# Kernel optimization log

Hardware: AMD Instinct MI355X
Metric: run time of the kernel (lower is better)

## Reference

```python
import jax, jax.numpy as jnp
import numpy as np

NUM_HEADS = 4
SCALE = 0.1767766952966369  # head_dim**-0.5, head_dim=32


def setup_inputs() -> dict:
    key = jax.random.key(0)
    k1, k2, k3 = jax.random.split(key, 3)
    B, N, C = 4096, 49, 384  # B = 64 images * 64 windows, N = 7*7, C = 3*embed_dims
    qkv = jax.random.normal(k1, (B, N, C), dtype=jnp.float32)
    mask = jax.random.normal(k2, (NUM_HEADS, N, N), dtype=jnp.float32)
    rotate_mask = jax.random.normal(k3, (64, N, N), dtype=jnp.float32)  # nW = 64
    hw_pad = jnp.array([56, 56], dtype=jnp.int32)  # metadata only, unused in math
    return {"qkv": qkv, "mask": mask, "rotate_mask": rotate_mask, "hw_pad": hw_pad}


def reference(qkv, mask, rotate_mask, hw_pad):
    B, N, C = qkv.shape
    H = NUM_HEADS
    hd = C // H // 3
    # [B,N,3,H,hd] -> [3,B,H,N,hd]
    qkv_r = qkv.reshape(B, N, 3, H, hd).transpose(2, 0, 3, 1, 4)
    q, k, v = qkv_r[0] * SCALE, qkv_r[1], qkv_r[2]
    attn = jnp.einsum('bhqd,bhkd->bhqk', q, k) + mask  # mask broadcasts over B
    nW = rotate_mask.shape[0]
    # shifted-window mask: add per-window rotate mask, broadcast over image batch and heads
    attn = attn.reshape(B // nW, nW, H, N, N) + rotate_mask[None, :, None, :, :]
    attn = jax.nn.softmax(attn.reshape(B, H, N, N), axis=-1)
    out = jnp.einsum('bhqk,bhkd->bhqd', attn, v)  # [B,H,N,hd]
    return out.transpose(0, 2, 1, 3).reshape(B, N, C // 3)
```

## Files before the change

### kernel.cpp

```cpp
#include <hip/hip_runtime.h>

#define NTOK 49
#define NH 4
#define HD 32
#define CIN 384
#define NW 64
#define NPAD 64
#define SCALE_F 0.1767766952966369f

typedef _Float16 f16x8 __attribute__((ext_vector_type(8)));
typedef float f32x16 __attribute__((ext_vector_type(16)));
typedef __fp16 fp16x2 __attribute__((ext_vector_type(2)));

__device__ __forceinline__ unsigned int pkh(float a, float b) {
    fp16x2 h = __builtin_amdgcn_cvt_pkrtz(a, b);
    return __builtin_bit_cast(unsigned int, h);
}

__global__ __launch_bounds__(64) void prep_cmask(
    const float* __restrict__ mask,
    const float* __restrict__ rot,
    float* __restrict__ cmT)
{
    const int wh = blockIdx.x;
    const int w = wh >> 2, h = wh & 3;
    const int i = threadIdx.x;
    for (int j = 0; j < NPAD; ++j) {
        float v;
        if (j >= NTOK) v = -1e30f;
        else if (i >= NTOK) v = 0.f;
        else v = mask[(h * NTOK + i) * NTOK + j] + rot[(w * NTOK + i) * NTOK + j];
        cmT[((size_t)wh * NPAD + j) * NPAD + i] = v;
    }
}

template<bool USE_CM>
__global__ __launch_bounds__(64) void win_attn_mfma(
    const float* __restrict__ qkv,
    const float* __restrict__ mask,
    const float* __restrict__ rot,
    const float* __restrict__ cmT,
    float* __restrict__ out)
{
    const int h = blockIdx.x & 3;
    const int b = blockIdx.x >> 2;
    const int w = b & (NW - 1);
    const int lane = threadIdx.x;
    const int l31 = lane & 31;
    const int hl = lane >> 5;

    __shared__ _Float16 Qs[NPAD * HD];
    __shared__ _Float16 Ks[NPAD * HD];

    const float* base = qkv + (size_t)b * (NTOK * CIN) + h * HD;

    #pragma unroll
    for (int t8 = 0; t8 < 8; ++t8) {
        const int idx = lane + t8 * 64;
        const int n = idx >> 3;
        const int c = idx & 7;
        float4 fq = make_float4(0.f, 0.f, 0.f, 0.f);
        float4 fk = fq;
        if (n < NTOK) {
            const float* p = base + n * CIN + c * 4;
            fq = *reinterpret_cast<const float4*>(p);
            fk = *reinterpret_cast<const float4*>(p + 128);
        }
        uint2 uq, uk;
        uq.x = pkh(fq.x * SCALE_F, fq.y * SCALE_F);
        uq.y = pkh(fq.z * SCALE_F, fq.w * SCALE_F);
        uk.x = pkh(fk.x, fk.y);
        uk.y = pkh(fk.z, fk.w);
        *reinterpret_cast<uint2*>(&Qs[n * HD + c * 4]) = uq;
        *reinterpret_cast<uint2*>(&Ks[n * HD + c * 4]) = uk;
    }

    float cm[2][2][16];
    #pragma unroll
    for (int it = 0; it < 2; ++it) {
        #pragma unroll
        for (int jt = 0; jt < 2; ++jt) {
            #pragma unroll
            for (int r = 0; r < 16; ++r) {
                const int j = (r & 3) + 8 * (r >> 2) + 4 * hl + 32 * jt;
                const int i = l31 + 32 * it;
                if (USE_CM) {
                    cm[it][jt][r] = cmT[((size_t)(w * 4 + h) * NPAD + j) * NPAD + i];
                } else {
                    float v;
                    if (j >= NTOK) v = -1e30f;
                    else if (i >= NTOK) v = 0.f;
                    else v = mask[(h * NTOK + i) * NTOK + j] + rot[(w * NTOK + i) * NTOK + j];
                    cm[it][jt][r] = v;
                }
            }
        }
    }

    __syncthreads();

    f16x8 ka[2][2], qa[2][2];
    #pragma unroll
    for (int t = 0; t < 2; ++t) {
        #pragma unroll
        for (int ks = 0; ks < 2; ++ks) {
            ka[t][ks] = *reinterpret_cast<const f16x8*>(&Ks[(l31 + 32 * t) * HD + ks * 16 + hl * 8]);
            qa[t][ks] = *reinterpret_cast<const f16x8*>(&Qs[(l31 + 32 * t) * HD + ks * 16 + hl * 8]);
        }
    }

    f32x16 acc[2][2];
    #pragma unroll
    for (int it = 0; it < 2; ++it) {
        #pragma unroll
        for (int jt = 0; jt < 2; ++jt) {
            f32x16 a;
            #pragma unroll
            for (int r = 0; r < 16; ++r) a[r] = 0.f;
            a = __builtin_amdgcn_mfma_f32_32x32x16_f16(ka[jt][0], qa[it][0], a, 0, 0, 0);
            a = __builtin_amdgcn_mfma_f32_32x32x16_f16(ka[jt][1], qa[it][1], a, 0, 0, 0);
            acc[it][jt] = a;
        }
    }

    #pragma unroll
    for (int it = 0; it < 2; ++it) {
        float m = -3e38f;
        #pragma unroll
        for (int jt = 0; jt < 2; ++jt) {
            #pragma unroll
            for (int r = 0; r < 16; ++r) {
                acc[it][jt][r] += cm[it][jt][r];
                m = fmaxf(m, acc[it][jt][r]);
            }
        }
        m = fmaxf(m, __shfl_xor(m, 32));
        float s = 0.f;
        #pragma unroll
        for (int jt = 0; jt < 2; ++jt) {
            #pragma unroll
            for (int r = 0; r < 16; ++r) {
                const float e = __expf(acc[it][jt][r] - m);
                acc[it][jt][r] = e;
                s += e;
            }
        }
        s += __shfl_xor(s, 32);
        const float inv = 1.f / s;
        #pragma unroll
        for (int jt = 0; jt < 2; ++jt) {
            #pragma unroll
            for (int r = 0; r < 16; ++r)
                acc[it][jt][r] *= inv;
        }
    }

    f32x16 oacc[2];
    #pragma unroll
    for (int it = 0; it < 2; ++it) {
        #pragma unroll
        for (int r = 0; r < 16; ++r) oacc[it][r] = 0.f;
    }

    #pragma unroll
    for (int ks = 0; ks < 4; ++ks) {
        unsigned int vd[4];
        #pragma unroll
        for (int ep = 0; ep < 4; ++ep) {
            const int j0 = 16 * ks + 8 * hl + 2 * ep;
            float v0 = 0.f, v1 = 0.f;
            if (j0 < NTOK)
                v0 = qkv[((size_t)b * NTOK + j0) * CIN + 256 + h * HD + l31];
            if (j0 + 1 < NTOK)
                v1 = qkv[((size_t)b * NTOK + j0 + 1) * CIN + 256 + h * HD + l31];
            vd[ep] = pkh(v0, v1);
        }
        uint4 vu = make_uint4(vd[0], vd[1], vd[2], vd[3]);
        const f16x8 vb = __builtin_bit_cast(f16x8, vu);

        const int jt = ks >> 1;
        const int r8 = 8 * (ks & 1);
        #pragma unroll
        for (int it = 0; it < 2; ++it) {
            const unsigned int lo0 = pkh(acc[it][jt][r8 + 0], acc[it][jt][r8 + 1]);
            const unsigned int lo1 = pkh(acc[it][jt][r8 + 2], acc[it][jt][r8 + 3]);
            const unsigned int hi0 = pkh(acc[it][jt][r8 + 4], acc[it][jt][r8 + 5]);
            const unsigned int hi1 = pkh(acc[it][jt][r8 + 6], acc[it][jt][r8 + 7]);
            const unsigned int x0 = hl ? lo0 : hi0;
            const unsigned int x1 = hl ? lo1 : hi1;
            const unsigned int y0 = (unsigned int)__shfl_xor((int)x0, 32);
            const unsigned int y1 = (unsigned int)__shfl_xor((int)x1, 32);
            uint4 pu;
            pu.x = hl ? y0 : lo0;
            pu.y = hl ? y1 : lo1;
            pu.z = hl ? hi0 : y0;
            pu.w = hl ? hi1 : y1;
            const f16x8 pa = __builtin_bit_cast(f16x8, pu);
            oacc[it] = __builtin_amdgcn_mfma_f32_32x32x16_f16(pa, vb, oacc[it], 0, 0, 0);
        }
    }

    #pragma unroll
    for (int it = 0; it < 2; ++it) {
        #pragma unroll
        for (int r = 0; r < 16; ++r) {
            const int i = (r & 3) + 8 * (r >> 2) + 4 * hl + 32 * it;
            if (i < NTOK)
                out[((size_t)b * NTOK + i) * (NH * HD) + h * HD + l31] = oacc[it][r];
        }
    }
}

extern "C" void kernel_launch(void* const* d_in, const int* in_sizes, int n_in,
                              void* d_out, int out_size, void* d_ws, size_t ws_size,
                              hipStream_t stream) {
    const float* qkv  = (const float*)d_in[0];
    const float* mask = (const float*)d_in[1];
    const float* rot  = (const float*)d_in[2];
    float* out = (float*)d_out;

    const int Btot = in_sizes[0] / (NTOK * CIN);
    dim3 grid(Btot * NH);

    const size_t cm_bytes = (size_t)NW * NH * NPAD * NPAD * sizeof(float);
    if (ws_size >= cm_bytes && d_ws != nullptr) {
        float* cmT = (float*)d_ws;
        prep_cmask<<<dim3(NW * NH), 64, 0, stream>>>(mask, rot, cmT);
        win_attn_mfma<true><<<grid, 64, 0, stream>>>(qkv, mask, rot, cmT, out);
    } else {
        win_attn_mfma<false><<<grid, 64, 0, stream>>>(qkv, mask, rot, nullptr, out);
    }
}
```

Baseline: 112.2 us.

## Restructure attention per row-tile loop, vectorize combined-mask loads, prefetch V early

The combined mask is now stored row-major, so each lane reads its mask values with float4 loads instead of scattered scalar loads from a transposed layout. The attention body becomes a non-unrolled loop over the two query row tiles, which keeps only one tile's scores and mask in registers at a time and cuts register pressure. V is loaded and packed to fp16 before the barrier so the global loads overlap the Q/K staging, and MFMA sections get raised wave priority. The cost is that the two row tiles now run one after the other instead of being interleaved, which reduces instruction-level parallelism.

```diff
diff --git a/kernel.cpp b/kernel.cpp
--- a/kernel.cpp
+++ b/kernel.cpp
@@ -20,17 +20,17 @@
 __global__ __launch_bounds__(64) void prep_cmask(
     const float* __restrict__ mask,
     const float* __restrict__ rot,
-    float* __restrict__ cmT)
+    float* __restrict__ cmM)
 {
     const int wh = blockIdx.x;
     const int w = wh >> 2, h = wh & 3;
-    const int i = threadIdx.x;
-    for (int j = 0; j < NPAD; ++j) {
+    const int j = threadIdx.x;
+    for (int i = 0; i < NPAD; ++i) {
         float v;
         if (j >= NTOK) v = -1e30f;
         else if (i >= NTOK) v = 0.f;
         else v = mask[(h * NTOK + i) * NTOK + j] + rot[(w * NTOK + i) * NTOK + j];
-        cmT[((size_t)wh * NPAD + j) * NPAD + i] = v;
+        cmM[((size_t)wh * NPAD + i) * NPAD + j] = v;
     }
 }
 
@@ -39,7 +39,7 @@
     const float* __restrict__ qkv,
     const float* __restrict__ mask,
     const float* __restrict__ rot,
-    const float* __restrict__ cmT,
+    const float* __restrict__ cmM,
     float* __restrict__ out)
 {
     const int h = blockIdx.x & 3;
@@ -75,63 +75,89 @@
         *reinterpret_cast<uint2*>(&Ks[n * HD + c * 4]) = uk;
     }
 
-    float cm[2][2][16];
+    uint4 vb[4];
+    {
+        const float* vbase = qkv + (size_t)b * (NTOK * CIN) + 256 + h * HD + l31;
+        #pragma unroll
+        for (int ks = 0; ks < 4; ++ks) {
+            unsigned dd[4];
+            #pragma unroll
+            for (int ep = 0; ep < 4; ++ep) {
+                const int j0 = 16 * ks + 8 * hl + 2 * ep;
+                const float v0 = (j0     < NTOK) ? vbase[(size_t)j0 * CIN]       : 0.f;
+                const float v1 = (j0 + 1 < NTOK) ? vbase[(size_t)(j0 + 1) * CIN] : 0.f;
+                dd[ep] = pkh(v0, v1);
+            }
+            vb[ks] = make_uint4(dd[0], dd[1], dd[2], dd[3]);
+        }
+    }
+
+    __syncthreads();
+
+    f16x8 ka[2][2];
     #pragma unroll
+    for (int t = 0; t < 2; ++t) {
+        #pragma unroll
+        for (int ks = 0; ks < 2; ++ks) {
+            ka[t][ks] = *reinterpret_cast<const f16x8*>(&Ks[(l31 + 32 * t) * HD + ks * 16 + hl * 8]);
+        }
+    }
+
+    #pragma unroll 1
     for (int it = 0; it < 2; ++it) {
-        #pragma unroll
-        for (int jt = 0; jt < 2; ++jt) {
-            #pragma unroll
-            for (int r = 0; r < 16; ++r) {
-                const int j = (r & 3) + 8 * (r >> 2) + 4 * hl + 32 * jt;
-                const int i = l31 + 32 * it;
-                if (USE_CM) {
-                    cm[it][jt][r] = cmT[((size_t)(w * 4 + h) * NPAD + j) * NPAD + i];
-                } else {
+        const int i = l31 + 32 * it;
+        const f16x8 qa0 = *reinterpret_cast<const f16x8*>(&Qs[i * HD + hl * 8]);
+        const f16x8 qa1 = *reinterpret_cast<const f16x8*>(&Qs[i * HD + 16 + hl * 8]);
+
+        float cmv[2][16];
+        if (USE_CM) {
+            const float* cmRow = cmM + ((size_t)(w * 4 + h) * NPAD + i) * NPAD;
+            #pragma unroll
+            for (int jt = 0; jt < 2; ++jt) {
+                #pragma unroll
+                for (int rq = 0; rq < 4; ++rq) {
+                    const float4 c = *reinterpret_cast<const float4*>(&cmRow[32 * jt + 8 * rq + 4 * hl]);
+                    cmv[jt][4 * rq + 0] = c.x;
+                    cmv[jt][4 * rq + 1] = c.y;
+                    cmv[jt][4 * rq + 2] = c.z;
+                    cmv[jt][4 * rq + 3] = c.w;
+                }
+            }
+        } else {
+            #pragma unroll
+            for (int jt = 0; jt < 2; ++jt) {
+                #pragma unroll
+                for (int r = 0; r < 16; ++r) {
+                    const int j = (r & 3) + 8 * (r >> 2) + 4 * hl + 32 * jt;
                     float v;
                     if (j >= NTOK) v = -1e30f;
                     else if (i >= NTOK) v = 0.f;
                     else v = mask[(h * NTOK + i) * NTOK + j] + rot[(w * NTOK + i) * NTOK + j];
-                    cm[it][jt][r] = v;
+                    cmv[jt][r] = v;
                 }
             }
         }
-    }
-
-    __syncthreads();
-
-    f16x8 ka[2][2], qa[2][2];
-    #pragma unroll
-    for (int t = 0; t < 2; ++t) {
-        #pragma unroll
-        for (int ks = 0; ks < 2; ++ks) {
-            ka[t][ks] = *reinterpret_cast<const f16x8*>(&Ks[(l31 + 32 * t) * HD + ks * 16 + hl * 8]);
-            qa[t][ks] = *reinterpret_cast<const f16x8*>(&Qs[(l31 + 32 * t) * HD + ks * 16 + hl * 8]);
-        }
-    }
-
-    f32x16 acc[2][2];
-    #pragma unroll
-    for (int it = 0; it < 2; ++it) {
+
+        f32x16 acc[2];
+        __builtin_amdgcn_s_setprio(1);
         #pragma unroll
         for (int jt = 0; jt < 2; ++jt) {
             f32x16 a;
             #pragma unroll
             for (int r = 0; r < 16; ++r) a[r] = 0.f;
-            a = __builtin_amdgcn_mfma_f32_32x32x16_f16(ka[jt][0], qa[it][0], a, 0, 0, 0);
-            a = __builtin_amdgcn_mfma_f32_32x32x16_f16(ka[jt][1], qa[it][1], a, 0, 0, 0);
-            acc[it][jt] = a;
-        }
-    }
-
-    #pragma unroll
-    for (int it = 0; it < 2; ++it) {
+            a = __builtin_amdgcn_mfma_f32_32x32x16_f16(ka[jt][0], qa0, a, 0, 0, 0);
+            a = __builtin_amdgcn_mfma_f32_32x32x16_f16(ka[jt][1], qa1, a, 0, 0, 0);
+            acc[jt] = a;
+        }
+        __builtin_amdgcn_s_setprio(0);
+
         float m = -3e38f;
         #pragma unroll
         for (int jt = 0; jt < 2; ++jt) {
             #pragma unroll
             for (int r = 0; r < 16; ++r) {
-                acc[it][jt][r] += cm[it][jt][r];
-                m = fmaxf(m, acc[it][jt][r]);
+                acc[jt][r] += cmv[jt][r];
+                m = fmaxf(m, acc[jt][r]);
             }
         }
         m = fmaxf(m, __shfl_xor(m, 32));
@@ -140,8 +166,8 @@
         for (int jt = 0; jt < 2; ++jt) {
             #pragma unroll
             for (int r = 0; r < 16; ++r) {
-                const float e = __expf(acc[it][jt][r] - m);
-                acc[it][jt][r] = e;
+                const float e = __expf(acc[jt][r] - m);
+                acc[jt][r] = e;
                 s += e;
             }
         }
@@ -150,63 +176,40 @@
         #pragma unroll
         for (int jt = 0; jt < 2; ++jt) {
             #pragma unroll
-            for (int r = 0; r < 16; ++r)
-                acc[it][jt][r] *= inv;
-        }
-    }
-
-    f32x16 oacc[2];
-    #pragma unroll
-    for (int it = 0; it < 2; ++it) {
-        #pragma unroll
-        for (int r = 0; r < 16; ++r) oacc[it][r] = 0.f;
-    }
-
-    #pragma unroll
-    for (int ks = 0; ks < 4; ++ks) {
-        unsigned int vd[4];
-        #pragma unroll
-        for (int ep = 0; ep < 4; ++ep) {
-            const int j0 = 16 * ks + 8 * hl + 2 * ep;
-            float v0 = 0.f, v1 = 0.f;
-            if (j0 < NTOK)
-                v0 = qkv[((size_t)b * NTOK + j0) * CIN + 256 + h * HD + l31];
-            if (j0 + 1 < NTOK)
-                v1 = qkv[((size_t)b * NTOK + j0 + 1) * CIN + 256 + h * HD + l31];
-            vd[ep] = pkh(v0, v1);
-        }
-        uint4 vu = make_uint4(vd[0], vd[1], vd[2], vd[3]);
-        const f16x8 vb = __builtin_bit_cast(f16x8, vu);
-
-        const int jt = ks >> 1;
-        const int r8 = 8 * (ks & 1);
-        #pragma unroll
-        for (int it = 0; it < 2; ++it) {
-            const unsigned int lo0 = pkh(acc[it][jt][r8 + 0], acc[it][jt][r8 + 1]);
-            const unsigned int lo1 = pkh(acc[it][jt][r8 + 2], acc[it][jt][r8 + 3]);
-            const unsigned int hi0 = pkh(acc[it][jt][r8 + 4], acc[it][jt][r8 + 5]);
-            const unsigned int hi1 = pkh(acc[it][jt][r8 + 6], acc[it][jt][r8 + 7]);
-            const unsigned int x0 = hl ? lo0 : hi0;
-            const unsigned int x1 = hl ? lo1 : hi1;
-            const unsigned int y0 = (unsigned int)__shfl_xor((int)x0, 32);
-            const unsigned int y1 = (unsigned int)__shfl_xor((int)x1, 32);
+            for (int r = 0; r < 16; ++r) acc[jt][r] *= inv;
+        }
+
+        f32x16 oacc;
+        #pragma unroll
+        for (int r = 0; r < 16; ++r) oacc[r] = 0.f;
+
+        #pragma unroll
+        for (int ks = 0; ks < 4; ++ks) {
+            const int jt = ks >> 1;
+            const int r8 = 8 * (ks & 1);
+            const unsigned lo0 = pkh(acc[jt][r8 + 0], acc[jt][r8 + 1]);
+            const unsigned lo1 = pkh(acc[jt][r8 + 2], acc[jt][r8 + 3]);
+            const unsigned hi0 = pkh(acc[jt][r8 + 4], acc[jt][r8 + 5]);
+            const unsigned hi1 = pkh(acc[jt][r8 + 6], acc[jt][r8 + 7]);
+            const unsigned x0 = hl ? lo0 : hi0;
+            const unsigned x1 = hl ? lo1 : hi1;
+            const unsigned y0 = (unsigned)__shfl_xor((int)x0, 32);
+            const unsigned y1 = (unsigned)__shfl_xor((int)x1, 32);
             uint4 pu;
             pu.x = hl ? y0 : lo0;
             pu.y = hl ? y1 : lo1;
             pu.z = hl ? hi0 : y0;
             pu.w = hl ? hi1 : y1;
-            const f16x8 pa = __builtin_bit_cast(f16x8, pu);
-            oacc[it] = __builtin_amdgcn_mfma_f32_32x32x16_f16(pa, vb, oacc[it], 0, 0, 0);
-        }
-    }
-
-    #pragma unroll
-    for (int it = 0; it < 2; ++it) {
+            const f16x8 pa  = __builtin_bit_cast(f16x8, pu);
+            const f16x8 vbk = __builtin_bit_cast(f16x8, vb[ks]);
+            oacc = __builtin_amdgcn_mfma_f32_32x32x16_f16(pa, vbk, oacc, 0, 0, 0);
+        }
+
+        float* obase = out + (size_t)b * NTOK * (NH * HD) + h * HD + l31;
         #pragma unroll
         for (int r = 0; r < 16; ++r) {
-            const int i = (r & 3) + 8 * (r >> 2) + 4 * hl + 32 * it;
-            if (i < NTOK)
-                out[((size_t)b * NTOK + i) * (NH * HD) + h * HD + l31] = oacc[it][r];
+            const int io = (r & 3) + 8 * (r >> 2) + 4 * hl + 32 * it;
+            if (io < NTOK) obase[(size_t)io * (NH * HD)] = oacc[r];
         }
     }
 }
@@ -224,9 +227,9 @@
 
     const size_t cm_bytes = (size_t)NW * NH * NPAD * NPAD * sizeof(float);
     if (ws_size >= cm_bytes && d_ws != nullptr) {
-        float* cmT = (float*)d_ws;
-        prep_cmask<<<dim3(NW * NH), 64, 0, stream>>>(mask, rot, cmT);
-        win_attn_mfma<true><<<grid, 64, 0, stream>>>(qkv, mask, rot, cmT, out);
+        float* cmM = (float*)d_ws;
+        prep_cmask<<<dim3(NW * NH), 64, 0, stream>>>(mask, rot, cmM);
+        win_attn_mfma<true><<<grid, 64, 0, stream>>>(qkv, mask, rot, cmM, out);
     } else {
         win_attn_mfma<false><<<grid, 64, 0, stream>>>(qkv, mask, rot, nullptr, out);
     }
```

After: 128.3 us. 1.14x slower.
